# Performance work log

Hardware: AMD Instinct MI355X
Metric: run time of the kernel (lower is better)

The kernel has to match this reference:

```python
import jax, jax.numpy as jnp
import numpy as np

N_NODES_PER_GRAPH = 64
NUM_GRAPHS = 2048
N = NUM_GRAPHS * N_NODES_PER_GRAPH  # 131072 total nodes
E = N * 8                           # 1048576 edges
IN_DIM, H1, H2 = 64, 128, 64
OUT_DIM = (N_NODES_PER_GRAPH * N_NODES_PER_GRAPH - N_NODES_PER_GRAPH) // 2  # 2016


def setup_inputs() -> dict:
    key = jax.random.key(0)
    ks = jax.random.split(key, 16)
    s = 0.05
    x = jax.random.normal(ks[0], (N, IN_DIM), dtype=jnp.float32)
    # edges within each graph: offsets within graph + graph base offset
    src_local = jax.random.randint(ks[1], (E,), 0, N_NODES_PER_GRAPH)
    dst_local = jax.random.randint(ks[2], (E,), 0, N_NODES_PER_GRAPH)
    gid = jnp.repeat(jnp.arange(NUM_GRAPHS), E // NUM_GRAPHS) * N_NODES_PER_GRAPH
    edge_index = jnp.stack([src_local + gid, dst_local + gid]).astype(jnp.int64)
    batch = jnp.repeat(jnp.arange(NUM_GRAPHS), N_NODES_PER_GRAPH).astype(jnp.int64)
    eps = jax.random.normal(ks[3], (NUM_GRAPHS, H2), dtype=jnp.float32)
    return {
        "x": x, "edge_index": edge_index, "batch": batch, "eps": eps,
        "w1_rel": jax.random.normal(ks[4], (IN_DIM, H1)) * s,
        "b1": jnp.zeros((H1,), jnp.float32),
        "w1_root": jax.random.normal(ks[5], (IN_DIM, H1)) * s,
        "w2_rel": jax.random.normal(ks[6], (H1, H2)) * s,
        "b2": jnp.zeros((H2,), jnp.float32),
        "w2_root": jax.random.normal(ks[7], (H1, H2)) * s,
        "w3_rel": jax.random.normal(ks[8], (H1, H2)) * s,
        "b3": jnp.zeros((H2,), jnp.float32),
        "w3_root": jax.random.normal(ks[9], (H1, H2)) * s,
        "fc1_w": jax.random.normal(ks[10], (H2, H1)) * s,
        "fc1_b": jnp.zeros((H1,), jnp.float32),
        "fc2_w": jax.random.normal(ks[11], (H1, OUT_DIM)) * s,
        "fc2_b": jnp.zeros((OUT_DIM,), jnp.float32),
    }


def _graph_conv(h, src, dst, w_rel, b, w_root):
    # PyG GraphConv: out_i = W_rel @ (sum_{j in N(i)} h_j) + b + W_root @ h_i
    agg = jax.ops.segment_sum(h[src], dst, num_segments=N)  # [N, d_in]
    return agg @ w_rel + b + h @ w_root


def _segment_mean(h, seg):
    s = jax.ops.segment_sum(h, seg, num_segments=NUM_GRAPHS)
    cnt = jax.ops.segment_sum(jnp.ones((h.shape[0],), h.dtype), seg, num_segments=NUM_GRAPHS)
    return s / jnp.maximum(cnt, 1.0)[:, None]


def reference(x, edge_index, batch, eps, w1_rel, b1, w1_root, w2_rel, b2, w2_root,
              w3_rel, b3, w3_root, fc1_w, fc1_b, fc2_w, fc2_b):
    src, dst = edge_index[0], edge_index[1]
    # encode (dropout p=0.0 -> identity)
    h1 = jax.nn.relu(_graph_conv(x, src, dst, w1_rel, b1, w1_root))
    mu = _segment_mean(_graph_conv(h1, src, dst, w2_rel, b2, w2_root), batch)
    logvar = _segment_mean(_graph_conv(h1, src, dst, w3_rel, b3, w3_root), batch)
    # reparameterize with provided eps
    z = mu + eps * jnp.exp(0.5 * logvar)
    # decode
    h = jax.nn.relu(z @ fc1_w + fc1_b)
    recon = jax.nn.sigmoid(h @ fc2_w + fc2_b)
    return recon, mu, logvar
```

## Files before the change

kernel.cpp:

```cpp
#include <hip/hip_runtime.h>
#include <math.h>

#define NG 2048
#define NPG 64
#define EPG 512
#define ETOT (NG*EPG)
#define IND 64
#define H1D 128
#define H2D 64
#define OUTD 2016

typedef __attribute__((ext_vector_type(8))) short bf16x8;
typedef __attribute__((ext_vector_type(4))) float f32x4;
typedef __attribute__((ext_vector_type(8))) unsigned short u16x8;
typedef __attribute__((ext_vector_type(4))) short s16x4;

__device__ inline short f2b(float f) {
  union { float f; unsigned u; } v; v.f = f;
  unsigned r = (v.u + 0x7FFFu + ((v.u >> 16) & 1u)) >> 16;
  return (short)r;
}

__global__ void p_w1(const float* __restrict__ w1_rel, const float* __restrict__ w1_root,
                     short* __restrict__ WTgF,
                     const float* __restrict__ w2_rel, const float* __restrict__ w2_root,
                     const float* __restrict__ w3_rel, const float* __restrict__ w3_root,
                     const float* __restrict__ fc1_w,
                     short* __restrict__ W23T, short* __restrict__ fc1T) {
  __shared__ float L[4224];
  const int b = blockIdx.x;
  const int tid = threadIdx.x;
  if (b < 8) {
    const int ct = b;
    const int ks = tid >> 6, l = tid & 63;
    const int col = ct*16 + (l & 15);
    const int kb  = ks*32 + (l >> 4)*8;
    short tmp[8];
    #pragma unroll
    for (int j = 0; j < 8; ++j) {
      const int k = kb + j;
      float v = (k < 64) ? w1_rel[k*H1D + col] : w1_root[(k - 64)*H1D + col];
      tmp[j] = f2b(v);
    }
    *(uint4*)&WTgF[(size_t)((ct*4 + ks)*64 + l)*8] = *(uint4*)tmp;
  } else if (b < 12) {
    const int cc = b - 8;
    const int j0 = cc*32;
    const float* wrel  = (cc < 2) ? w2_rel  : w3_rel;
    const float* wroot = (cc < 2) ? w2_root : w3_root;
    const int jl = j0 & 63;
    const int c = tid >> 3, k0 = (tid & 7)*32;
    for (int i = tid; i < 4096; i += 256) {
      int k = i >> 5, cc2 = i & 31;
      L[k*33 + cc2] = wrel[k*H2D + jl + cc2];
    }
    __syncthreads();
    if (k0 < 128)
      for (int kk = 0; kk < 32; ++kk)
        W23T[(size_t)(j0 + c)*264 + k0 + kk] = f2b(L[(k0 + kk)*33 + c]);
    __syncthreads();
    for (int i = tid; i < 4096; i += 256) {
      int k = i >> 5, cc2 = i & 31;
      L[k*33 + cc2] = wroot[k*H2D + jl + cc2];
    }
    __syncthreads();
    if (k0 >= 128)
      for (int kk = 0; kk < 32; ++kk)
        W23T[(size_t)(j0 + c)*264 + k0 + kk] = f2b(L[(k0 + kk - 128)*33 + c]);
  } else {
    const int c0 = (b - 12)*64;
    for (int i = tid; i < 4096; i += 256) {
      int k = i >> 6, c = i & 63;
      L[k*65 + c] = fc1_w[k*H1D + c0 + c];
    }
    __syncthreads();
    const int c = tid >> 2, k0 = (tid & 3)*16;
    for (int kk = 0; kk < 16; ++kk)
      fc1T[(size_t)(c0 + c)*72 + k0 + kk] = f2b(L[(k0 + kk)*65 + c]);
  }
}

__global__ __launch_bounds__(256, 5) void k1_enc(
    const float* __restrict__ x, const int* __restrict__ ei,
    const short* __restrict__ WTgF, const float* __restrict__ b1,
    short* __restrict__ SVb,
    const float* __restrict__ fc2_w, short* __restrict__ WF2g)
{
  __shared__ __align__(16) char smem[32000];
  const int g = blockIdx.x;
  const int tid = threadIdx.x;

  if (g >= NG) {
    float* L = (float*)smem;
    const int bid = g - NG;
    const int c0 = bid*32;
    for (int i = tid; i < 4096; i += 256) {
      int k = i >> 5, c = i & 31;
      L[k*33 + c] = fc2_w[(size_t)k*OUTD + c0 + c];
    }
    __syncthreads();
    const int tl = tid >> 7;
    const int r  = tid & 127;
    const int ks = r >> 5;
    const int lp = r & 31;
    const int ct = bid*2 + tl;
    #pragma unroll
    for (int u = 0; u < 2; ++u) {
      const int l = lp*2 + u;
      const int cl = tl*16 + (l & 15);
      const int kb = ks*32 + (l >> 4)*8;
      short tmp[8];
      #pragma unroll
      for (int j = 0; j < 8; ++j) tmp[j] = f2b(L[(kb + j)*33 + cl]);
      *(uint4*)&WF2g[(size_t)((ct*4 + ks)*64 + l)*8] = *(uint4*)tmp;
    }
    return;
  }

  short* Xb   = (short*)smem;
  short* XbT  = (short*)(smem + 9216);
  short* Ab   = (short*)(smem + 18432);
  unsigned* Au32 = (unsigned*)(smem + 27648);
  float* Dg   = (float*)(smem + 31744);

  const int w = tid >> 6, l = tid & 63;

  const int e0 = g*EPG + tid*2;
  const int2 sp = *(const int2*)&ei[e0];
  const int2 dp = *(const int2*)&ei[ETOT + e0];
  const int s0 = sp.x & 63, d0 = dp.x & 63;
  const int s1 = sp.y & 63, d1 = dp.y & 63;
  const int n = tid >> 2, f0 = (tid & 3) * 16;
  const float* xr = x + (size_t)g*(NPG*IND) + n*IND + f0;
  float4 v0 = *(const float4*)&xr[0];
  float4 v1 = *(const float4*)&xr[4];
  float4 v2 = *(const float4*)&xr[8];
  float4 v3 = *(const float4*)&xr[12];

  for (int i = tid; i < 64*16; i += 256) Au32[i] = 0u;
  __syncthreads();

  atomicAdd(&Au32[d0*16 + (s0 >> 2)], 1u << (8*(s0 & 3)));
  atomicAdd(&Au32[d1*16 + (s1 >> 2)], 1u << (8*(s1 & 3)));

  {
    u16x8 lo, hi;
    lo[0]=(unsigned short)f2b(v0.x); lo[1]=(unsigned short)f2b(v0.y);
    lo[2]=(unsigned short)f2b(v0.z); lo[3]=(unsigned short)f2b(v0.w);
    lo[4]=(unsigned short)f2b(v1.x); lo[5]=(unsigned short)f2b(v1.y);
    lo[6]=(unsigned short)f2b(v1.z); lo[7]=(unsigned short)f2b(v1.w);
    hi[0]=(unsigned short)f2b(v2.x); hi[1]=(unsigned short)f2b(v2.y);
    hi[2]=(unsigned short)f2b(v2.z); hi[3]=(unsigned short)f2b(v2.w);
    hi[4]=(unsigned short)f2b(v3.x); hi[5]=(unsigned short)f2b(v3.y);
    hi[6]=(unsigned short)f2b(v3.z); hi[7]=(unsigned short)f2b(v3.w);
    *(u16x8*)&Xb[n*72 + f0]     = lo;
    *(u16x8*)&Xb[n*72 + f0 + 8] = hi;
    #pragma unroll
    for (int j = 0; j < 8; ++j) {
      XbT[(f0 + j)*72 + n]     = (short)lo[j];
      XbT[(f0 + 8 + j)*72 + n] = (short)hi[j];
    }
  }
  __syncthreads();

  {
    const int row = tid >> 2, qw = tid & 3;
    unsigned wds[4];
    #pragma unroll
    for (int q = 0; q < 4; ++q) wds[q] = Au32[row*16 + qw*4 + q];
    auto pk = [](unsigned wv, int p) -> unsigned {
      unsigned c0 = (wv >> (16*p)) & 255u, c1 = (wv >> (16*p + 8)) & 255u;
      return (unsigned)(unsigned short)f2b((float)c0)
           | ((unsigned)(unsigned short)f2b((float)c1) << 16);
    };
    uint4 oA = { pk(wds[0],0), pk(wds[0],1), pk(wds[1],0), pk(wds[1],1) };
    uint4 oB = { pk(wds[2],0), pk(wds[2],1), pk(wds[3],0), pk(wds[3],1) };
    unsigned* abp = (unsigned*)&Ab[row*72 + qw*16];
    *(uint4*)&abp[0] = oA;
    *(uint4*)&abp[4] = oB;
  }

  {
    const int squad = tid >> 4;
    const int db = (tid & 15) * 4;
    unsigned ps = 0;
    #pragma unroll
    for (int i = 0; i < 4; ++i) ps += Au32[(db + i)*16 + squad];
    ps += __shfl_xor(ps, 1); ps += __shfl_xor(ps, 2);
    ps += __shfl_xor(ps, 4); ps += __shfl_xor(ps, 8);
    if ((tid & 15) == 0) {
      f32x4 dv = { (float)(ps & 255u), (float)((ps >> 8) & 255u),
                   (float)((ps >> 16) & 255u), (float)(ps >> 24) };
      *(f32x4*)&Dg[squad*4] = dv;
    }
  }

  const int rm = w*16;
  const int fr = l & 15;
  const int koff = (l >> 4) * 8;

  f32x4 agc[4];
  #pragma unroll
  for (int t = 0; t < 4; ++t) agc[t] = (f32x4){0.f,0.f,0.f,0.f};
  #pragma unroll
  for (int ks = 0; ks < 2; ++ks) {
    bf16x8 a = *(const bf16x8*)&Ab[(rm + fr)*72 + ks*32 + koff];
    #pragma unroll
    for (int t = 0; t < 4; ++t) {
      bf16x8 b = *(const bf16x8*)&XbT[(t*16 + fr)*72 + ks*32 + koff];
      agc[t] = __builtin_amdgcn_mfma_f32_16x16x32_bf16(a, b, agc[t], 0, 0, 0);
    }
  }

  bf16x8 bfr[2][4];
  #pragma unroll
  for (int ct2 = 0; ct2 < 2; ++ct2)
    #pragma unroll
    for (int ks = 0; ks < 4; ++ks)
      bfr[ct2][ks] = *(const bf16x8*)&WTgF[(size_t)(((2*w + ct2)*4 + ks)*64 + l)*8];

  short* AGb = Ab;
  #pragma unroll
  for (int t = 0; t < 4; ++t)
    #pragma unroll
    for (int r = 0; r < 4; ++r)
      AGb[(rm + (l>>4)*4 + r)*72 + t*16 + fr] = f2b(agc[t][r]);

  __syncthreads();

  const float bb0 = b1[(2*w)*16 + fr];
  const float bb1 = b1[(2*w + 1)*16 + fr];
  float hs0 = 0.f, ws0 = 0.f, hs1 = 0.f, ws1 = 0.f;
  #pragma unroll
  for (int rt = 0; rt < 4; ++rt) {
    bf16x8 afr[4];
    #pragma unroll
    for (int ks = 0; ks < 4; ++ks)
      afr[ks] = (ks < 2)
        ? *(const bf16x8*)&AGb[(rt*16 + fr)*72 + ks*32 + koff]
        : *(const bf16x8*)&Xb[(rt*16 + fr)*72 + (ks - 2)*32 + koff];
    f32x4 a0 = (f32x4){0.f,0.f,0.f,0.f}, a1 = (f32x4){0.f,0.f,0.f,0.f};
    #pragma unroll
    for (int ks = 0; ks < 4; ++ks) {
      a0 = __builtin_amdgcn_mfma_f32_16x16x32_bf16(afr[ks], bfr[0][ks], a0, 0, 0, 0);
      a1 = __builtin_amdgcn_mfma_f32_16x16x32_bf16(afr[ks], bfr[1][ks], a1, 0, 0, 0);
    }
    f32x4 dgv = *(const f32x4*)&Dg[rt*16 + (l >> 4)*4];
    #pragma unroll
    for (int r = 0; r < 4; ++r) {
      float va = fmaxf(a0[r] + bb0, 0.f);
      float vb = fmaxf(a1[r] + bb1, 0.f);
      hs0 += va; ws0 += dgv[r]*va;
      hs1 += vb; ws1 += dgv[r]*vb;
    }
  }
  hs0 += __shfl_down(hs0, 32); ws0 += __shfl_down(ws0, 32);
  hs1 += __shfl_down(hs1, 32); ws1 += __shfl_down(ws1, 32);
  hs0 += __shfl_down(hs0, 16); ws0 += __shfl_down(ws0, 16);
  hs1 += __shfl_down(hs1, 16); ws1 += __shfl_down(ws1, 16);
  if (l < 16) {
    short* svg = SVb + (size_t)g*256;
    svg[(2*w)*16 + l]           = f2b(ws0);
    svg[(2*w + 1)*16 + l]       = f2b(ws1);
    svg[128 + (2*w)*16 + l]     = f2b(hs0);
    svg[128 + (2*w + 1)*16 + l] = f2b(hs1);
  }
}

__global__ __launch_bounds__(256) void k1b_latent(
    const short* __restrict__ SVb, const short* __restrict__ W23T,
    const float* __restrict__ b2, const float* __restrict__ b3,
    const float* __restrict__ eps, const short* __restrict__ fc1T,
    const float* __restrict__ fc1_b,
    float* __restrict__ out_mu, float* __restrict__ out_lv, short* __restrict__ hbufF)
{
  __shared__ short SV[32*264];
  __shared__ short Zt[32*72];
  const int g0 = blockIdx.x * 32;
  const int tid = threadIdx.x;
  const int w = tid >> 6, l = tid & 63;
  const int s = w >> 1;
  const int h = w & 1;
  const int fr = l & 15;
  const int koff = (l >> 4) * 8;

  for (int i = tid; i < 32*64; i += 256) {
    const int r = i >> 6, kq = (i & 63)*4;
    *(s16x4*)&SV[r*264 + kq] = *(const s16x4*)&SVb[(size_t)(g0 + r)*256 + kq];
  }
  __syncthreads();

  f32x4 acc[4];
  #pragma unroll
  for (int t = 0; t < 4; ++t) acc[t] = (f32x4){0.f,0.f,0.f,0.f};
  #pragma unroll
  for (int ks = 0; ks < 8; ++ks) {
    bf16x8 a = *(const bf16x8*)&SV[(s*16 + fr)*264 + ks*32 + koff];
    #pragma unroll
    for (int j = 0; j < 2; ++j) {
      bf16x8 bm = *(const bf16x8*)&W23T[((2*h + j)*16 + fr)*264 + ks*32 + koff];
      bf16x8 bl = *(const bf16x8*)&W23T[((2*h + j + 4)*16 + fr)*264 + ks*32 + koff];
      acc[j]     = __builtin_amdgcn_mfma_f32_16x16x32_bf16(a, bm, acc[j], 0, 0, 0);
      acc[2 + j] = __builtin_amdgcn_mfma_f32_16x16x32_bf16(a, bl, acc[2 + j], 0, 0, 0);
    }
  }
  #pragma unroll
  for (int j = 0; j < 2; ++j) {
    const int col = (2*h + j)*16 + fr;
    const float bb2 = b2[col], bb3 = b3[col];
    #pragma unroll
    for (int r = 0; r < 4; ++r) {
      const int row = s*16 + (l>>4)*4 + r;
      const size_t gg = (size_t)(g0 + row);
      float mu = acc[j][r]     * (1.f/64.f) + bb2;
      float lv = acc[2 + j][r] * (1.f/64.f) + bb3;
      out_mu[gg*64 + col] = mu;
      out_lv[gg*64 + col] = lv;
      float z = mu + eps[gg*64 + col] * __expf(0.5f*lv);
      Zt[row*72 + col] = f2b(z);
    }
  }
  __syncthreads();

  f32x4 hacc[4];
  #pragma unroll
  for (int t = 0; t < 4; ++t) hacc[t] = (f32x4){0.f,0.f,0.f,0.f};
  #pragma unroll
  for (int ks = 0; ks < 2; ++ks) {
    bf16x8 a = *(const bf16x8*)&Zt[(s*16 + fr)*72 + ks*32 + koff];
    #pragma unroll
    for (int j = 0; j < 4; ++j) {
      bf16x8 b = *(const bf16x8*)&fc1T[((h*4 + j)*16 + fr)*72 + ks*32 + koff];
      hacc[j] = __builtin_amdgcn_mfma_f32_16x16x32_bf16(a, b, hacc[j], 0, 0, 0);
    }
  }
  #pragma unroll
  for (int j = 0; j < 4; ++j) {
    const int col = (h*4 + j)*16 + fr;
    const int ks2 = col >> 5;
    const int q   = (col >> 3) & 3;
    const int j8  = col & 7;
    const float bb = fc1_b[col];
    #pragma unroll
    for (int r = 0; r < 4; ++r) {
      const int row = s*16 + (l>>4)*4 + r;
      const int rt2 = blockIdx.x*2 + (row >> 4);
      const int lane = (row & 15) + 16*q;
      hbufF[(size_t)((rt2*4 + ks2)*64 + lane)*8 + j8] = f2b(fmaxf(hacc[j][r] + bb, 0.f));
    }
  }
}

__global__ __launch_bounds__(256, 8) void k2_decoder(
    const short* __restrict__ hbufF, const short* __restrict__ WF2g,
    const float* __restrict__ fc2_b, float* __restrict__ recon)
{
  const int bx = blockIdx.x, by = blockIdx.y;
  const int tid = threadIdx.x;
  const int w = tid >> 6, l = tid & 63;
  const int fr = l & 15;
  const int rt = bx*4 + w;

  bf16x8 afr[4];
  #pragma unroll
  for (int ks = 0; ks < 4; ++ks)
    afr[ks] = *(const bf16x8*)&hbufF[(size_t)((rt*4 + ks)*64 + l)*8];

  f32x4 acc[6];
  #pragma unroll
  for (int t = 0; t < 6; ++t) acc[t] = (f32x4){0.f,0.f,0.f,0.f};

  #pragma unroll
  for (int ks = 0; ks < 4; ++ks) {
    #pragma unroll
    for (int t = 0; t < 6; ++t) {
      const int ct = by*6 + t;
      bf16x8 b = *(const bf16x8*)&WF2g[(size_t)((ct*4 + ks)*64 + l)*8];
      acc[t] = __builtin_amdgcn_mfma_f32_16x16x32_bf16(afr[ks], b, acc[t], 0, 0, 0);
    }
  }

  #pragma unroll
  for (int t = 0; t < 6; ++t) {
    const int col = by*96 + t*16 + fr;
    const float bb = fc2_b[col];
    #pragma unroll
    for (int r = 0; r < 4; ++r) {
      const int row = bx*64 + w*16 + (l>>4)*4 + r;
      float v = acc[t][r] + bb;
      recon[(size_t)row*OUTD + col] = 1.f/(1.f + __expf(-v));
    }
  }
}

extern "C" void kernel_launch(void* const* d_in, const int* in_sizes, int n_in,
                              void* d_out, int out_size, void* d_ws, size_t ws_size,
                              hipStream_t stream) {
  const float* x       = (const float*)d_in[0];
  const int*   ei      = (const int*)d_in[1];
  const float* eps     = (const float*)d_in[3];
  const float* w1_rel  = (const float*)d_in[4];
  const float* b1      = (const float*)d_in[5];
  const float* w1_root = (const float*)d_in[6];
  const float* w2_rel  = (const float*)d_in[7];
  const float* b2      = (const float*)d_in[8];
  const float* w2_root = (const float*)d_in[9];
  const float* w3_rel  = (const float*)d_in[10];
  const float* b3      = (const float*)d_in[11];
  const float* w3_root = (const float*)d_in[12];
  const float* fc1_w   = (const float*)d_in[13];
  const float* fc1_b   = (const float*)d_in[14];
  const float* fc2_w   = (const float*)d_in[15];
  const float* fc2_b   = (const float*)d_in[16];

  float* recon  = (float*)d_out;
  float* out_mu = recon + (size_t)NG*OUTD;
  float* out_lv = out_mu + (size_t)NG*H2D;

  char* p = (char*)d_ws;
  short* WTgF  = (short*)p;              p += 8*4*64*8*2;
  short* WF2g  = (short*)p;              p += 126*4*64*8*2;
  short* fc1T  = (short*)p;              p += 128*72*2;
  short* W23T  = (short*)p;              p += 128*264*2;
  short* SVb   = (short*)p;              p += (size_t)NG*256*2;
  short* hbufF = (short*)p;

  p_w1<<<14, 256, 0, stream>>>(w1_rel, w1_root, WTgF,
                               w2_rel, w2_root, w3_rel, w3_root,
                               fc1_w, W23T, fc1T);
  k1_enc<<<NG + 63, 256, 0, stream>>>(x, ei, WTgF, b1, SVb, fc2_w, WF2g);
  k1b_latent<<<64, 256, 0, stream>>>(SVb, W23T, b2, b3, eps, fc1T, fc1_b,
                                     out_mu, out_lv, hbufF);
  k2_decoder<<<dim3(32, 21), 256, 0, stream>>>(hbufF, WF2g, fc2_b, recon);
}
```

Baseline: 137.9 us.

## Fuse latent and decoder kernels, move weight prep into encoder launch

Merges the latent kernel (mu/logvar, reparameterization, fc1) into the decoder so each block recomputes the small latent and fc1 stages for its 32 graphs and keeps the hidden activations in shared memory. This removes one launch and the global hbuf round trip. The W2/W3 and fc1 weight repacking moves from the first prep kernel into extra blocks of the encoder launch, and the decoder MFMA operands are swapped so each lane stores float4 of recon. The cost is that the latent/fc1 work is repeated across the 21 column blocks, and those blocks now wait on the encoder.

Measured after the change: 142.6 us. 3.4% more time.

```diff
diff --git a/kernel.cpp b/kernel.cpp
--- a/kernel.cpp
+++ b/kernel.cpp
@@ -22,69 +22,29 @@
 }
 
 __global__ void p_w1(const float* __restrict__ w1_rel, const float* __restrict__ w1_root,
-                     short* __restrict__ WTgF,
-                     const float* __restrict__ w2_rel, const float* __restrict__ w2_root,
-                     const float* __restrict__ w3_rel, const float* __restrict__ w3_root,
-                     const float* __restrict__ fc1_w,
-                     short* __restrict__ W23T, short* __restrict__ fc1T) {
-  __shared__ float L[4224];
-  const int b = blockIdx.x;
-  const int tid = threadIdx.x;
-  if (b < 8) {
-    const int ct = b;
-    const int ks = tid >> 6, l = tid & 63;
-    const int col = ct*16 + (l & 15);
-    const int kb  = ks*32 + (l >> 4)*8;
-    short tmp[8];
-    #pragma unroll
-    for (int j = 0; j < 8; ++j) {
-      const int k = kb + j;
-      float v = (k < 64) ? w1_rel[k*H1D + col] : w1_root[(k - 64)*H1D + col];
-      tmp[j] = f2b(v);
-    }
-    *(uint4*)&WTgF[(size_t)((ct*4 + ks)*64 + l)*8] = *(uint4*)tmp;
-  } else if (b < 12) {
-    const int cc = b - 8;
-    const int j0 = cc*32;
-    const float* wrel  = (cc < 2) ? w2_rel  : w3_rel;
-    const float* wroot = (cc < 2) ? w2_root : w3_root;
-    const int jl = j0 & 63;
-    const int c = tid >> 3, k0 = (tid & 7)*32;
-    for (int i = tid; i < 4096; i += 256) {
-      int k = i >> 5, cc2 = i & 31;
-      L[k*33 + cc2] = wrel[k*H2D + jl + cc2];
-    }
-    __syncthreads();
-    if (k0 < 128)
-      for (int kk = 0; kk < 32; ++kk)
-        W23T[(size_t)(j0 + c)*264 + k0 + kk] = f2b(L[(k0 + kk)*33 + c]);
-    __syncthreads();
-    for (int i = tid; i < 4096; i += 256) {
-      int k = i >> 5, cc2 = i & 31;
-      L[k*33 + cc2] = wroot[k*H2D + jl + cc2];
-    }
-    __syncthreads();
-    if (k0 >= 128)
-      for (int kk = 0; kk < 32; ++kk)
-        W23T[(size_t)(j0 + c)*264 + k0 + kk] = f2b(L[(k0 + kk - 128)*33 + c]);
-  } else {
-    const int c0 = (b - 12)*64;
-    for (int i = tid; i < 4096; i += 256) {
-      int k = i >> 6, c = i & 63;
-      L[k*65 + c] = fc1_w[k*H1D + c0 + c];
-    }
-    __syncthreads();
-    const int c = tid >> 2, k0 = (tid & 3)*16;
-    for (int kk = 0; kk < 16; ++kk)
-      fc1T[(size_t)(c0 + c)*72 + k0 + kk] = f2b(L[(k0 + kk)*65 + c]);
-  }
+                     short* __restrict__ WTgF) {
+  const int ct = blockIdx.x;
+  const int ks = threadIdx.x >> 6, l = threadIdx.x & 63;
+  const int col = ct*16 + (l & 15);
+  const int kb  = ks*32 + (l >> 4)*8;
+  short tmp[8];
+  #pragma unroll
+  for (int j = 0; j < 8; ++j) {
+    const int k = kb + j;
+    float v = (k < 64) ? w1_rel[k*H1D + col] : w1_root[(k - 64)*H1D + col];
+    tmp[j] = f2b(v);
+  }
+  *(uint4*)&WTgF[(size_t)((ct*4 + ks)*64 + l)*8] = *(uint4*)tmp;
 }
 
 __global__ __launch_bounds__(256, 5) void k1_enc(
     const float* __restrict__ x, const int* __restrict__ ei,
     const short* __restrict__ WTgF, const float* __restrict__ b1,
     short* __restrict__ SVb,
-    const float* __restrict__ fc2_w, short* __restrict__ WF2g)
+    const float* __restrict__ fc2_w, const float* __restrict__ w2_rel,
+    const float* __restrict__ w2_root, const float* __restrict__ w3_rel,
+    const float* __restrict__ w3_root, const float* __restrict__ fc1_w,
+    short* __restrict__ WF2g, short* __restrict__ W23T, short* __restrict__ fc1T)
 {
   __shared__ __align__(16) char smem[32000];
   const int g = blockIdx.x;
@@ -93,26 +53,62 @@
   if (g >= NG) {
     float* L = (float*)smem;
     const int bid = g - NG;
-    const int c0 = bid*32;
-    for (int i = tid; i < 4096; i += 256) {
-      int k = i >> 5, c = i & 31;
-      L[k*33 + c] = fc2_w[(size_t)k*OUTD + c0 + c];
-    }
-    __syncthreads();
-    const int tl = tid >> 7;
-    const int r  = tid & 127;
-    const int ks = r >> 5;
-    const int lp = r & 31;
-    const int ct = bid*2 + tl;
-    #pragma unroll
-    for (int u = 0; u < 2; ++u) {
-      const int l = lp*2 + u;
-      const int cl = tl*16 + (l & 15);
-      const int kb = ks*32 + (l >> 4)*8;
-      short tmp[8];
+    if (bid < 63) {
+      const int c0 = bid*32;
+      for (int i = tid; i < 4096; i += 256) {
+        int k = i >> 5, c = i & 31;
+        L[k*33 + c] = fc2_w[(size_t)k*OUTD + c0 + c];
+      }
+      __syncthreads();
+      const int tl = tid >> 7;
+      const int r  = tid & 127;
+      const int ks = r >> 5;
+      const int lp = r & 31;
+      const int ct = bid*2 + tl;
       #pragma unroll
-      for (int j = 0; j < 8; ++j) tmp[j] = f2b(L[(kb + j)*33 + cl]);
-      *(uint4*)&WF2g[(size_t)((ct*4 + ks)*64 + l)*8] = *(uint4*)tmp;
+      for (int u = 0; u < 2; ++u) {
+        const int l = lp*2 + u;
+        const int cl = tl*16 + (l & 15);
+        const int kb = ks*32 + (l >> 4)*8;
+        short tmp[8];
+        #pragma unroll
+        for (int j = 0; j < 8; ++j) tmp[j] = f2b(L[(kb + j)*33 + cl]);
+        *(uint4*)&WF2g[(size_t)((ct*4 + ks)*64 + l)*8] = *(uint4*)tmp;
+      }
+    } else if (bid < 67) {
+      const int cc = bid - 63;
+      const int j0 = cc*32;
+      const float* wrel  = (cc < 2) ? w2_rel  : w3_rel;
+      const float* wroot = (cc < 2) ? w2_root : w3_root;
+      const int jl = j0 & 63;
+      const int c = tid >> 3, k0 = (tid & 7)*32;
+      for (int i = tid; i < 4096; i += 256) {
+        int k = i >> 5, cc2 = i & 31;
+        L[k*33 + cc2] = wrel[k*H2D + jl + cc2];
+      }
+      __syncthreads();
+      if (k0 < 128)
+        for (int kk = 0; kk < 32; ++kk)
+          W23T[(size_t)(j0 + c)*264 + k0 + kk] = f2b(L[(k0 + kk)*33 + c]);
+      __syncthreads();
+      for (int i = tid; i < 4096; i += 256) {
+        int k = i >> 5, cc2 = i & 31;
+        L[k*33 + cc2] = wroot[k*H2D + jl + cc2];
+      }
+      __syncthreads();
+      if (k0 >= 128)
+        for (int kk = 0; kk < 32; ++kk)
+          W23T[(size_t)(j0 + c)*264 + k0 + kk] = f2b(L[(k0 + kk - 128)*33 + c]);
+    } else {
+      const int c0 = (bid - 67)*64;
+      for (int i = tid; i < 4096; i += 256) {
+        int k = i >> 6, c = i & 63;
+        L[k*65 + c] = fc1_w[k*H1D + c0 + c];
+      }
+      __syncthreads();
+      const int c = tid >> 2, k0 = (tid & 3)*16;
+      for (int kk = 0; kk < 16; ++kk)
+        fc1T[(size_t)(c0 + c)*72 + k0 + kk] = f2b(L[(k0 + kk)*65 + c]);
     }
     return;
   }
@@ -267,16 +263,20 @@
   }
 }
 
-__global__ __launch_bounds__(256) void k1b_latent(
+__global__ __launch_bounds__(256) void k2_fused(
     const short* __restrict__ SVb, const short* __restrict__ W23T,
     const float* __restrict__ b2, const float* __restrict__ b3,
     const float* __restrict__ eps, const short* __restrict__ fc1T,
-    const float* __restrict__ fc1_b,
-    float* __restrict__ out_mu, float* __restrict__ out_lv, short* __restrict__ hbufF)
+    const float* __restrict__ fc1_b, const short* __restrict__ WF2g,
+    const float* __restrict__ fc2_b,
+    float* __restrict__ out_mu, float* __restrict__ out_lv,
+    float* __restrict__ recon)
 {
   __shared__ short SV[32*264];
   __shared__ short Zt[32*72];
+  __shared__ short Hs[32*136];
   const int g0 = blockIdx.x * 32;
+  const int by = blockIdx.y;
   const int tid = threadIdx.x;
   const int w = tid >> 6, l = tid & 63;
   const int s = w >> 1;
@@ -314,8 +314,10 @@
       const size_t gg = (size_t)(g0 + row);
       float mu = acc[j][r]     * (1.f/64.f) + bb2;
       float lv = acc[2 + j][r] * (1.f/64.f) + bb3;
-      out_mu[gg*64 + col] = mu;
-      out_lv[gg*64 + col] = lv;
+      if (by == 0) {
+        out_mu[gg*64 + col] = mu;
+        out_lv[gg*64 + col] = lv;
+      }
       float z = mu + eps[gg*64 + col] * __expf(0.5f*lv);
       Zt[row*72 + col] = f2b(z);
     }
@@ -337,59 +339,44 @@
   #pragma unroll
   for (int j = 0; j < 4; ++j) {
     const int col = (h*4 + j)*16 + fr;
-    const int ks2 = col >> 5;
-    const int q   = (col >> 3) & 3;
-    const int j8  = col & 7;
     const float bb = fc1_b[col];
     #pragma unroll
     for (int r = 0; r < 4; ++r) {
       const int row = s*16 + (l>>4)*4 + r;
-      const int rt2 = blockIdx.x*2 + (row >> 4);
-      const int lane = (row & 15) + 16*q;
-      hbufF[(size_t)((rt2*4 + ks2)*64 + lane)*8 + j8] = f2b(fmaxf(hacc[j][r] + bb, 0.f));
-    }
-  }
-}
-
-__global__ __launch_bounds__(256, 8) void k2_decoder(
-    const short* __restrict__ hbufF, const short* __restrict__ WF2g,
-    const float* __restrict__ fc2_b, float* __restrict__ recon)
-{
-  const int bx = blockIdx.x, by = blockIdx.y;
-  const int tid = threadIdx.x;
-  const int w = tid >> 6, l = tid & 63;
-  const int fr = l & 15;
-  const int rt = bx*4 + w;
-
-  bf16x8 afr[4];
+      Hs[row*136 + col] = f2b(fmaxf(hacc[j][r] + bb, 0.f));
+    }
+  }
+  __syncthreads();
+
+  bf16x8 ah[4];
   #pragma unroll
   for (int ks = 0; ks < 4; ++ks)
-    afr[ks] = *(const bf16x8*)&hbufF[(size_t)((rt*4 + ks)*64 + l)*8];
-
-  f32x4 acc[6];
-  #pragma unroll
-  for (int t = 0; t < 6; ++t) acc[t] = (f32x4){0.f,0.f,0.f,0.f};
-
+    ah[ks] = *(const bf16x8*)&Hs[(s*16 + fr)*136 + ks*32 + koff];
+
+  f32x4 dcc[3];
+  #pragma unroll
+  for (int t = 0; t < 3; ++t) dcc[t] = (f32x4){0.f,0.f,0.f,0.f};
   #pragma unroll
   for (int ks = 0; ks < 4; ++ks) {
     #pragma unroll
-    for (int t = 0; t < 6; ++t) {
-      const int ct = by*6 + t;
-      bf16x8 b = *(const bf16x8*)&WF2g[(size_t)((ct*4 + ks)*64 + l)*8];
-      acc[t] = __builtin_amdgcn_mfma_f32_16x16x32_bf16(afr[ks], b, acc[t], 0, 0, 0);
-    }
-  }
-
-  #pragma unroll
-  for (int t = 0; t < 6; ++t) {
-    const int col = by*96 + t*16 + fr;
-    const float bb = fc2_b[col];
-    #pragma unroll
-    for (int r = 0; r < 4; ++r) {
-      const int row = bx*64 + w*16 + (l>>4)*4 + r;
-      float v = acc[t][r] + bb;
-      recon[(size_t)row*OUTD + col] = 1.f/(1.f + __expf(-v));
-    }
+    for (int t = 0; t < 3; ++t) {
+      const int ct = by*6 + h*3 + t;
+      bf16x8 bw = *(const bf16x8*)&WF2g[(size_t)((ct*4 + ks)*64 + l)*8];
+      dcc[t] = __builtin_amdgcn_mfma_f32_16x16x32_bf16(bw, ah[ks], dcc[t], 0, 0, 0);
+    }
+  }
+
+  #pragma unroll
+  for (int t = 0; t < 3; ++t) {
+    const int colq = (by*6 + h*3 + t)*16 + (l >> 4)*4;
+    const int row  = g0 + s*16 + fr;
+    const float4 bb = *(const float4*)&fc2_b[colq];
+    float4 o;
+    o.x = 1.f/(1.f + __expf(-(dcc[t][0] + bb.x)));
+    o.y = 1.f/(1.f + __expf(-(dcc[t][1] + bb.y)));
+    o.z = 1.f/(1.f + __expf(-(dcc[t][2] + bb.z)));
+    o.w = 1.f/(1.f + __expf(-(dcc[t][3] + bb.w)));
+    *(float4*)&recon[(size_t)row*OUTD + colq] = o;
   }
 }
 
@@ -422,14 +409,11 @@
   short* WF2g  = (short*)p;              p += 126*4*64*8*2;
   short* fc1T  = (short*)p;              p += 128*72*2;
   short* W23T  = (short*)p;              p += 128*264*2;
-  short* SVb   = (short*)p;              p += (size_t)NG*256*2;
-  short* hbufF = (short*)p;
-
-  p_w1<<<14, 256, 0, stream>>>(w1_rel, w1_root, WTgF,
-                               w2_rel, w2_root, w3_rel, w3_root,
-                               fc1_w, W23T, fc1T);
-  k1_enc<<<NG + 63, 256, 0, stream>>>(x, ei, WTgF, b1, SVb, fc2_w, WF2g);
-  k1b_latent<<<64, 256, 0, stream>>>(SVb, W23T, b2, b3, eps, fc1T, fc1_b,
-                                     out_mu, out_lv, hbufF);
-  k2_decoder<<<dim3(32, 21), 256, 0, stream>>>(hbufF, WF2g, fc2_b, recon);
+  short* SVb   = (short*)p;
+
+  p_w1<<<8, 256, 0, stream>>>(w1_rel, w1_root, WTgF);
+  k1_enc<<<NG + 69, 256, 0, stream>>>(x, ei, WTgF, b1, SVb,
+      fc2_w, w2_rel, w2_root, w3_rel, w3_root, fc1_w, WF2g, W23T, fc1T);
+  k2_fused<<<dim3(64, 21), 256, 0, stream>>>(SVb, W23T, b2, b3, eps, fc1T, fc1_b,
+                                             WF2g, fc2_b, out_mu, out_lv, recon);
 }
```
